# Kernel tuning notes

Hardware: AMD Instinct MI355X
Metric: run time of the kernel (lower is better)

The kernel has to match this reference:

```python
import jax, jax.numpy as jnp
import numpy as np

N_NODES = 50000
D = 128
N_EDGES = 600000


def setup_inputs() -> dict:
    key = jax.random.key(0)
    k1, k2, k3, k4 = jax.random.split(key, 4)
    x = jax.random.normal(k1, (N_NODES, D), dtype=jnp.float32)
    edge_index = jax.random.randint(k2, (2, N_EDGES), 0, N_NODES, dtype=jnp.int64)
    # edge MLP params: Linear(2D -> D) -> ReLU -> Linear(D -> D)
    W1 = jax.random.normal(k3, (2 * D, D), dtype=jnp.float32) * (1.0 / np.sqrt(2 * D))
    b1 = jnp.zeros((D,), dtype=jnp.float32)
    W2 = jax.random.normal(k4, (D, D), dtype=jnp.float32) * (1.0 / np.sqrt(D))
    b2 = jnp.zeros((D,), dtype=jnp.float32)
    return {"x": x, "edge_index": edge_index, "W1": W1, "b1": b1, "W2": W2, "b2": b2}


def reference(x, edge_index, W1, b1, W2, b2):
    # gather sender / receiver node features and concat along feature dim
    src = x[edge_index[0]]            # [E, D]
    dst = x[edge_index[1]]            # [E, D]
    edge_inputs = jnp.concatenate([src, dst], axis=1)  # [E, 2D]
    # edge MLP (model_fn)
    h = jax.nn.relu(edge_inputs @ W1 + b1)             # [E, D]
    edge_attr = h @ W2 + b2                            # [E, D]
    return edge_attr
```

## Files before the change

kernel.cpp:

```cpp
#include <hip/hip_runtime.h>

typedef __attribute__((ext_vector_type(8))) short  short8;
typedef __attribute__((ext_vector_type(4))) float  float4v;
typedef __attribute__((ext_vector_type(4))) int    int4v;

#define E_TILE 64
#define LDH    136
#define PGRID  768

#define BAR_LGKM asm volatile("s_waitcnt lgkmcnt(0)\n\ts_barrier" ::: "memory")

__device__ __forceinline__ short f2bf(float f) {
    union { float f; unsigned u; } v; v.f = f;
    unsigned r = (v.u + 0x7FFFu + ((v.u >> 16) & 1u)) >> 16;
    return (short)r;
}

__global__ __launch_bounds__(256)
void cvt_x_kernel(const float* __restrict__ x, short* __restrict__ x16, long n8) {
    long i = (long)blockIdx.x * 256 + threadIdx.x;
    if (i >= n8) return;
    const float4v* p = (const float4v*)(x + i * 8);
    float4v a = p[0], b = p[1];
    unsigned r0, r1, r2, r3;
    asm("v_cvt_pk_bf16_f32 %0, %1, %2" : "=v"(r0) : "v"(a.x), "v"(a.y));
    asm("v_cvt_pk_bf16_f32 %0, %1, %2" : "=v"(r1) : "v"(a.z), "v"(a.w));
    asm("v_cvt_pk_bf16_f32 %0, %1, %2" : "=v"(r2) : "v"(b.x), "v"(b.y));
    asm("v_cvt_pk_bf16_f32 %0, %1, %2" : "=v"(r3) : "v"(b.z), "v"(b.w));
    int4v o; o.x = (int)r0; o.y = (int)r1; o.z = (int)r2; o.w = (int)r3;
    *(int4v*)(x16 + i * 8) = o;
}

__global__ __launch_bounds__(256, 3)
void edge_mlp_kernel(const short* __restrict__ x16,
                     const int*   __restrict__ ei,
                     const float* __restrict__ W1,
                     const float* __restrict__ b1,
                     const float* __restrict__ W2,
                     const float* __restrict__ b2,
                     float*       __restrict__ out,
                     int E, int nTiles) {
    __shared__ short sA[E_TILE * 256];
    __shared__ short sH[E_TILE * LDH];
    __shared__ int   sIdx[2][2 * E_TILE];

    const int tid  = threadIdx.x;
    const int wave = tid >> 6;
    const int lane = tid & 63;
    const int quad = lane >> 4;
    const int l16  = lane & 15;
    const int nBase = wave * 32;
    const int G = gridDim.x;

    short8 bw1[8][2];
    short8 bw2[4][2];
    #pragma unroll
    for (int kt = 0; kt < 8; ++kt)
        #pragma unroll
        for (int nt = 0; nt < 2; ++nt) {
            short8 f;
            #pragma unroll
            for (int j = 0; j < 8; ++j)
                f[j] = f2bf(W1[(kt * 32 + quad * 8 + j) * 128 + nBase + nt * 16 + l16]);
            bw1[kt][nt] = f;
        }
    #pragma unroll
    for (int kt = 0; kt < 4; ++kt)
        #pragma unroll
        for (int nt = 0; nt < 2; ++nt) {
            short8 f;
            #pragma unroll
            for (int j = 0; j < 8; ++j)
                f[j] = f2bf(W2[(kt * 32 + quad * 8 + j) * 128 + nBase + nt * 16 + l16]);
            bw2[kt][nt] = f;
        }
    float b1v[2], b2v[2];
    #pragma unroll
    for (int nt = 0; nt < 2; ++nt) {
        b1v[nt] = b1[nBase + nt * 16 + l16];
        b2v[nt] = b2[nBase + nt * 16 + l16];
    }

    auto stageIdx = [&](int b, int t) {
        if (tid < E_TILE) {
            int s = 0, d = 0;
            if (t < nTiles) {
                long eg = (long)t * E_TILE + tid;
                if (eg < (long)E) { s = ei[eg]; d = ei[(long)E + eg]; }
            }
            sIdx[b][tid] = s;
            sIdx[b][E_TILE + tid] = d;
        }
    };

    auto gather = [&](int b) {
        #pragma unroll
        for (int r = 0; r < 8; ++r) {
            int lin = tid + 256 * r;
            int row = lin >> 5;
            int cl  = lin & 31;
            int c   = cl ^ (row & 7);
            int node = (c < 16) ? sIdx[b][row] : sIdx[b][E_TILE + row];
            const short* gp = x16 + (long)node * 128 + (c & 15) * 8;
            __builtin_amdgcn_global_load_lds(
                (const __attribute__((address_space(1))) void*)gp,
                (__attribute__((address_space(3))) void*)&sA[lin * 8],
                16, 0, 0);
        }
    };

    const int t0 = blockIdx.x;
    if (t0 >= nTiles) return;
    stageIdx(0, t0);
    __syncthreads();
    gather(0);
    stageIdx(1, t0 + G);
    __syncthreads();

    int p = 1;
    for (int t = t0; t < nTiles; t += G) {
        const long eBase = (long)t * E_TILE;

        float4v acc[4][2];
        #pragma unroll
        for (int mt = 0; mt < 4; ++mt)
            #pragma unroll
            for (int nt = 0; nt < 2; ++nt)
                acc[mt][nt] = (float4v)(0.0f);

        #pragma unroll
        for (int kt = 0; kt < 8; ++kt) {
            short8 a[4];
            #pragma unroll
            for (int mt = 0; mt < 4; ++mt) {
                int row = mt * 16 + l16;
                int cl  = (kt * 4 + quad) ^ (l16 & 7);
                a[mt] = *(const short8*)&sA[row * 256 + cl * 8];
            }
            #pragma unroll
            for (int mt = 0; mt < 4; ++mt)
                #pragma unroll
                for (int nt = 0; nt < 2; ++nt)
                    acc[mt][nt] = __builtin_amdgcn_mfma_f32_16x16x32_bf16(
                        a[mt], bw1[kt][nt], acc[mt][nt], 0, 0, 0);
        }

        #pragma unroll
        for (int mt = 0; mt < 4; ++mt)
            #pragma unroll
            for (int nt = 0; nt < 2; ++nt)
                #pragma unroll
                for (int r = 0; r < 4; ++r) {
                    int m = mt * 16 + quad * 4 + r;
                    int n = nBase + nt * 16 + l16;
                    float h = fmaxf(acc[mt][nt][r] + b1v[nt], 0.0f);
                    sH[m * LDH + n] = f2bf(h);
                }

        BAR_LGKM;

        if (t + G < nTiles) gather(p);
        stageIdx(p ^ 1, t + 2 * G);

        float4v acc2[4][2];
        #pragma unroll
        for (int mt = 0; mt < 4; ++mt)
            #pragma unroll
            for (int nt = 0; nt < 2; ++nt)
                acc2[mt][nt] = (float4v)(0.0f);

        #pragma unroll
        for (int kt = 0; kt < 4; ++kt) {
            short8 a[4];
            #pragma unroll
            for (int mt = 0; mt < 4; ++mt)
                a[mt] = *(const short8*)&sH[(mt * 16 + l16) * LDH + kt * 32 + quad * 8];
            #pragma unroll
            for (int mt = 0; mt < 4; ++mt)
                #pragma unroll
                for (int nt = 0; nt < 2; ++nt)
                    acc2[mt][nt] = __builtin_amdgcn_mfma_f32_16x16x32_bf16(
                        a[mt], bw2[kt][nt], acc2[mt][nt], 0, 0, 0);
        }

        BAR_LGKM;

        {
            float* sHf = (float*)sH;
            const int slab = wave * 1088;
            #pragma unroll
            for (int ph = 0; ph < 2; ++ph) {
                #pragma unroll
                for (int mh = 0; mh < 2; ++mh) {
                    int mt = 2 * ph + mh;
                    #pragma unroll
                    for (int nt = 0; nt < 2; ++nt)
                        #pragma unroll
                        for (int r = 0; r < 4; ++r) {
                            int row = mh * 16 + quad * 4 + r;
                            int c   = nt * 16 + l16;
                            sHf[slab + row * 34 + c] = acc2[mt][nt][r] + b2v[nt];
                        }
                }
                #pragma unroll
                for (int i = 0; i < 4; ++i) {
                    int f   = lane + 64 * i;
                    int row = f >> 3;
                    int c   = f & 7;
                    float4v v = *(const float4v*)&sHf[slab + row * 34 + c * 4];
                    long e = eBase + 32 * ph + row;
                    if (e < (long)E)
                        __builtin_nontemporal_store(
                            v, (float4v*)&out[e * 128 + nBase + c * 4]);
                }
            }
        }

        __syncthreads();
        p ^= 1;
    }
}

extern "C" void kernel_launch(void* const* d_in, const int* in_sizes, int n_in,
                              void* d_out, int out_size, void* d_ws, size_t ws_size,
                              hipStream_t stream) {
    const float* x  = (const float*)d_in[0];
    const int*   ei = (const int*)d_in[1];
    const float* W1 = (const float*)d_in[2];
    const float* b1 = (const float*)d_in[3];
    const float* W2 = (const float*)d_in[4];
    const float* b2 = (const float*)d_in[5];
    float* out = (float*)d_out;
    short* x16 = (short*)d_ws;

    long n8 = (long)in_sizes[0] / 8;
    int cgrid = (int)((n8 + 255) / 256);
    cvt_x_kernel<<<cgrid, 256, 0, stream>>>(x, x16, n8);

    int E = in_sizes[1] / 2;
    int nTiles = (E + E_TILE - 1) / E_TILE;
    int grid = nTiles < PGRID ? nTiles : PGRID;
    edge_mlp_kernel<<<grid, 256, 0, stream>>>(x16, ei, W1, b1, W2, b2, out, E, nTiles);
}
```

Before: 473.8 us.

## Double-buffer gathered node tiles in LDS and reuse buffer for hidden/output staging

Replaces the single A buffer plus separate H buffer with two A buffers, so the gather for the next tile is issued at the start of the current tile and overlaps both MLP layers. The hidden activations and output staging are written back into the current A buffer using XOR-swizzled layouts instead of padded strides. The loop is unrolled over the two buffers, MFMA sections get raised wave priority, and a vmcnt-based barrier replaces the full sync. Occupancy drops to 2 blocks per CU and the persistent grid shrinks to 512 blocks; the x conversion store becomes nontemporal. The main risk is that lower occupancy and the partial vmcnt wait leave less latency hiding than before.

```diff
diff --git a/kernel.cpp b/kernel.cpp
--- a/kernel.cpp
+++ b/kernel.cpp
@@ -5,10 +5,10 @@
 typedef __attribute__((ext_vector_type(4))) int    int4v;
 
 #define E_TILE 64
-#define LDH    136
-#define PGRID  768
+#define PGRID  512
 
 #define BAR_LGKM asm volatile("s_waitcnt lgkmcnt(0)\n\ts_barrier" ::: "memory")
+#define BAR_VM8  asm volatile("s_waitcnt vmcnt(8) lgkmcnt(0)\n\ts_barrier" ::: "memory")
 
 __device__ __forceinline__ short f2bf(float f) {
     union { float f; unsigned u; } v; v.f = f;
@@ -28,10 +28,10 @@
     asm("v_cvt_pk_bf16_f32 %0, %1, %2" : "=v"(r2) : "v"(b.x), "v"(b.y));
     asm("v_cvt_pk_bf16_f32 %0, %1, %2" : "=v"(r3) : "v"(b.z), "v"(b.w));
     int4v o; o.x = (int)r0; o.y = (int)r1; o.z = (int)r2; o.w = (int)r3;
-    *(int4v*)(x16 + i * 8) = o;
-}
-
-__global__ __launch_bounds__(256, 3)
+    __builtin_nontemporal_store(o, (int4v*)(x16 + i * 8));
+}
+
+__global__ __launch_bounds__(256, 2)
 void edge_mlp_kernel(const short* __restrict__ x16,
                      const int*   __restrict__ ei,
                      const float* __restrict__ W1,
@@ -40,8 +40,8 @@
                      const float* __restrict__ b2,
                      float*       __restrict__ out,
                      int E, int nTiles) {
-    __shared__ short sA[E_TILE * 256];
-    __shared__ short sH[E_TILE * LDH];
+    __shared__ short sA0[E_TILE * 256];
+    __shared__ short sA1[E_TILE * 256];
     __shared__ int   sIdx[2][2 * E_TILE];
 
     const int tid  = threadIdx.x;
@@ -93,7 +93,7 @@
         }
     };
 
-    auto gather = [&](int b) {
+    auto gather = [&](auto& dstA, int b) {
         #pragma unroll
         for (int r = 0; r < 8; ++r) {
             int lin = tid + 256 * r;
@@ -104,120 +104,134 @@
             const short* gp = x16 + (long)node * 128 + (c & 15) * 8;
             __builtin_amdgcn_global_load_lds(
                 (const __attribute__((address_space(1))) void*)gp,
-                (__attribute__((address_space(3))) void*)&sA[lin * 8],
+                (__attribute__((address_space(3))) void*)&dstA[lin * 8],
                 16, 0, 0);
         }
+    };
+
+    auto tile_body = [&](auto& curA, auto& nxtA, int idxR, int idxW, int t) {
+        const long eBase = (long)t * E_TILE;
+
+        stageIdx(idxW, t + 2 * G);
+        const bool hasNext = (t + G < nTiles);
+        if (hasNext) gather(nxtA, idxR);
+        __builtin_amdgcn_sched_barrier(0);
+
+        float4v acc[4][2];
+        #pragma unroll
+        for (int mt = 0; mt < 4; ++mt)
+            #pragma unroll
+            for (int nt = 0; nt < 2; ++nt)
+                acc[mt][nt] = (float4v)(0.0f);
+
+        __builtin_amdgcn_s_setprio(1);
+        #pragma unroll
+        for (int kt = 0; kt < 8; ++kt) {
+            short8 a[4];
+            #pragma unroll
+            for (int mt = 0; mt < 4; ++mt) {
+                int row = mt * 16 + l16;
+                int cl  = (kt * 4 + quad) ^ (l16 & 7);
+                a[mt] = *(const short8*)&curA[row * 256 + cl * 8];
+            }
+            #pragma unroll
+            for (int mt = 0; mt < 4; ++mt)
+                #pragma unroll
+                for (int nt = 0; nt < 2; ++nt)
+                    acc[mt][nt] = __builtin_amdgcn_mfma_f32_16x16x32_bf16(
+                        a[mt], bw1[kt][nt], acc[mt][nt], 0, 0, 0);
+        }
+        __builtin_amdgcn_s_setprio(0);
+
+        BAR_LGKM;
+
+        #pragma unroll
+        for (int mt = 0; mt < 4; ++mt)
+            #pragma unroll
+            for (int nt = 0; nt < 2; ++nt) {
+                int hcb = wave * 4 + nt * 2 + (l16 >> 3);
+                #pragma unroll
+                for (int r = 0; r < 4; ++r) {
+                    int m = mt * 16 + quad * 4 + r;
+                    float h = fmaxf(acc[mt][nt][r] + b1v[nt], 0.0f);
+                    curA[m * 128 + ((hcb ^ (m & 7)) << 3) + (l16 & 7)] = f2bf(h);
+                }
+            }
+
+        BAR_LGKM;
+
+        float4v acc2[4][2];
+        #pragma unroll
+        for (int mt = 0; mt < 4; ++mt)
+            #pragma unroll
+            for (int nt = 0; nt < 2; ++nt)
+                acc2[mt][nt] = (float4v)(0.0f);
+
+        __builtin_amdgcn_s_setprio(1);
+        #pragma unroll
+        for (int kt = 0; kt < 4; ++kt) {
+            short8 a[4];
+            #pragma unroll
+            for (int mt = 0; mt < 4; ++mt) {
+                int m = mt * 16 + l16;
+                int hc = kt * 4 + quad;
+                a[mt] = *(const short8*)&curA[m * 128 + ((hc ^ (l16 & 7)) << 3)];
+            }
+            #pragma unroll
+            for (int mt = 0; mt < 4; ++mt)
+                #pragma unroll
+                for (int nt = 0; nt < 2; ++nt)
+                    acc2[mt][nt] = __builtin_amdgcn_mfma_f32_16x16x32_bf16(
+                        a[mt], bw2[kt][nt], acc2[mt][nt], 0, 0, 0);
+        }
+        __builtin_amdgcn_s_setprio(0);
+
+        float* slab = (float*)(&curA[0]) + 4096 + wave * 1024;
+        #pragma unroll
+        for (int ph = 0; ph < 2; ++ph) {
+            #pragma unroll
+            for (int mh = 0; mh < 2; ++mh)
+                #pragma unroll
+                for (int nt = 0; nt < 2; ++nt) {
+                    int c4 = nt * 4 + (l16 >> 2);
+                    #pragma unroll
+                    for (int r = 0; r < 4; ++r) {
+                        int row = mh * 16 + quad * 4 + r;
+                        slab[row * 32 + ((c4 ^ (row & 7)) << 2) + (l16 & 3)] =
+                            acc2[2 * ph + mh][nt][r] + b2v[nt];
+                    }
+                }
+            #pragma unroll
+            for (int i = 0; i < 4; ++i) {
+                int f   = lane + 64 * i;
+                int row = f >> 3;
+                int c4  = f & 7;
+                float4v v = *(const float4v*)&slab[row * 32 + ((c4 ^ (row & 7)) << 2)];
+                long e = eBase + 32 * ph + row;
+                if (e < (long)E)
+                    __builtin_nontemporal_store(
+                        v, (float4v*)&out[e * 128 + nBase + c4 * 4]);
+            }
+        }
+
+        BAR_VM8;
     };
 
     const int t0 = blockIdx.x;
     if (t0 >= nTiles) return;
     stageIdx(0, t0);
-    __syncthreads();
-    gather(0);
     stageIdx(1, t0 + G);
     __syncthreads();
-
-    int p = 1;
-    for (int t = t0; t < nTiles; t += G) {
-        const long eBase = (long)t * E_TILE;
-
-        float4v acc[4][2];
-        #pragma unroll
-        for (int mt = 0; mt < 4; ++mt)
-            #pragma unroll
-            for (int nt = 0; nt < 2; ++nt)
-                acc[mt][nt] = (float4v)(0.0f);
-
-        #pragma unroll
-        for (int kt = 0; kt < 8; ++kt) {
-            short8 a[4];
-            #pragma unroll
-            for (int mt = 0; mt < 4; ++mt) {
-                int row = mt * 16 + l16;
-                int cl  = (kt * 4 + quad) ^ (l16 & 7);
-                a[mt] = *(const short8*)&sA[row * 256 + cl * 8];
-            }
-            #pragma unroll
-            for (int mt = 0; mt < 4; ++mt)
-                #pragma unroll
-                for (int nt = 0; nt < 2; ++nt)
-                    acc[mt][nt] = __builtin_amdgcn_mfma_f32_16x16x32_bf16(
-                        a[mt], bw1[kt][nt], acc[mt][nt], 0, 0, 0);
-        }
-
-        #pragma unroll
-        for (int mt = 0; mt < 4; ++mt)
-            #pragma unroll
-            for (int nt = 0; nt < 2; ++nt)
-                #pragma unroll
-                for (int r = 0; r < 4; ++r) {
-                    int m = mt * 16 + quad * 4 + r;
-                    int n = nBase + nt * 16 + l16;
-                    float h = fmaxf(acc[mt][nt][r] + b1v[nt], 0.0f);
-                    sH[m * LDH + n] = f2bf(h);
-                }
-
-        BAR_LGKM;
-
-        if (t + G < nTiles) gather(p);
-        stageIdx(p ^ 1, t + 2 * G);
-
-        float4v acc2[4][2];
-        #pragma unroll
-        for (int mt = 0; mt < 4; ++mt)
-            #pragma unroll
-            for (int nt = 0; nt < 2; ++nt)
-                acc2[mt][nt] = (float4v)(0.0f);
-
-        #pragma unroll
-        for (int kt = 0; kt < 4; ++kt) {
-            short8 a[4];
-            #pragma unroll
-            for (int mt = 0; mt < 4; ++mt)
-                a[mt] = *(const short8*)&sH[(mt * 16 + l16) * LDH + kt * 32 + quad * 8];
-            #pragma unroll
-            for (int mt = 0; mt < 4; ++mt)
-                #pragma unroll
-                for (int nt = 0; nt < 2; ++nt)
-                    acc2[mt][nt] = __builtin_amdgcn_mfma_f32_16x16x32_bf16(
-                        a[mt], bw2[kt][nt], acc2[mt][nt], 0, 0, 0);
-        }
-
-        BAR_LGKM;
-
-        {
-            float* sHf = (float*)sH;
-            const int slab = wave * 1088;
-            #pragma unroll
-            for (int ph = 0; ph < 2; ++ph) {
-                #pragma unroll
-                for (int mh = 0; mh < 2; ++mh) {
-                    int mt = 2 * ph + mh;
-                    #pragma unroll
-                    for (int nt = 0; nt < 2; ++nt)
-                        #pragma unroll
-                        for (int r = 0; r < 4; ++r) {
-                            int row = mh * 16 + quad * 4 + r;
-                            int c   = nt * 16 + l16;
-                            sHf[slab + row * 34 + c] = acc2[mt][nt][r] + b2v[nt];
-                        }
-                }
-                #pragma unroll
-                for (int i = 0; i < 4; ++i) {
-                    int f   = lane + 64 * i;
-                    int row = f >> 3;
-                    int c   = f & 7;
-                    float4v v = *(const float4v*)&sHf[slab + row * 34 + c * 4];
-                    long e = eBase + 32 * ph + row;
-                    if (e < (long)E)
-                        __builtin_nontemporal_store(
-                            v, (float4v*)&out[e * 128 + nBase + c * 4]);
-                }
-            }
-        }
-
-        __syncthreads();
-        p ^= 1;
+    gather(sA0, 0);
+    __syncthreads();
+
+    int t = t0;
+    while (t < nTiles) {
+        tile_body(sA0, sA1, 1, 0, t);
+        t += G;
+        if (t >= nTiles) break;
+        tile_body(sA1, sA0, 0, 1, t);
+        t += G;
     }
 }
 
```

New measurement: 437.6 us. -7.6%, faster.
